# Performance work log

Hardware: AMD Instinct MI355X
Metric: run time of the kernel (lower is better)

Reference implementation:

```python
import jax, jax.numpy as jnp
from jax import lax
import numpy as np

B, T, U, M = 256, 256, 512, 64


def setup_inputs() -> dict:
    key = jax.random.key(0)
    ks = jax.random.split(key, 4)
    scale = 0.05
    return {
        "x": jax.random.normal(ks[0], (B, T, U), dtype=jnp.float32),
        "memory0": jnp.zeros((B, M * U), dtype=jnp.float32),
        "Wr": jax.random.normal(ks[1], (U, M + 1), dtype=jnp.float32) * scale,
        "br": jnp.zeros((M + 1,), dtype=jnp.float32),
        "Wt": jax.random.normal(ks[2], (U, U), dtype=jnp.float32) * scale,
        "bt": jnp.zeros((U,), dtype=jnp.float32),
        "Ww": jax.random.normal(ks[3], (U, M), dtype=jnp.float32) * scale,
        "bw": jnp.zeros((M,), dtype=jnp.float32),
    }


def reference(x, memory0, Wr, br, Wt, bt, Ww, bw):
    b, t, u = x.shape
    m = Ww.shape[1]
    mem0 = memory0.reshape(b, m, u)

    def step(mem, xt):
        # mem: [B, M, U], xt: [B, U]
        attended_mem = jnp.concatenate([mem, xt[:, None, :]], axis=1)  # [B, M+1, U]
        read_w = jax.nn.softmax(jnp.mean(attended_mem, axis=1) @ Wr + br, axis=-1)  # [B, M+1]
        attended = jnp.einsum('bm,bmu->bu', read_w, attended_mem)  # [B, U]
        transformed = jax.nn.relu(attended @ Wt + bt)  # [B, U]
        write_w = jax.nn.sigmoid(transformed @ Ww + bw)[:, :, None]  # [B, M, 1]
        mem = (1.0 - write_w) * mem + write_w * transformed[:, None, :]
        return mem, transformed

    _, outs = lax.scan(step, mem0, jnp.swapaxes(x, 0, 1))  # outs: [T, B, U]
    return jnp.swapaxes(outs, 0, 1)  # [B, T, U]
```

## Files before the change

### kernel.cpp

```cpp
#include <hip/hip_runtime.h>
#include <cstddef>

#define BB 256
#define TT 256
#define UU 512
#define MM 64
#define NT 512
#define NCACHE 12

typedef _Float16 h2 __attribute__((ext_vector_type(2)));
typedef unsigned int uint32;

#define NWTP (UU / 2 * UU)
#define NWWP (UU / 2 * MM)
#define NWRP (UU / 2 * MM)

__device__ __forceinline__ uint32 pkf(float lo, float hi) {
    h2 v; v[0] = (_Float16)lo; v[1] = (_Float16)hi;
    return __builtin_bit_cast(uint32, v);
}
__device__ __forceinline__ h2 toh2(uint32 u) { return __builtin_bit_cast(h2, u); }
__device__ __forceinline__ float fd2(uint32 wu, uint32 au, float acc) {
    return __builtin_amdgcn_fdot2(toh2(wu), toh2(au), acc, false);
}

__device__ __forceinline__ void bar() {
    asm volatile("s_waitcnt lgkmcnt(0)" ::: "memory");
    __builtin_amdgcn_s_barrier();
}
__device__ __forceinline__ void cfence() {
    asm volatile("" ::: "memory");
}

__global__ void cvt_kernel(const float* __restrict__ Wt,
                           const float* __restrict__ Wr,
                           const float* __restrict__ Ww,
                           uint32* __restrict__ Wtp,
                           uint32* __restrict__ Wwp,
                           uint32* __restrict__ Wrp) {
    int i = blockIdx.x * blockDim.x + threadIdx.x;
    const int n = NWTP + NWWP + NWRP;
    for (; i < n; i += gridDim.x * blockDim.x) {
        if (i < NWTP) {
            int k2 = i >> 9, r = i & 511;
            int jj = r >> 3, c = r & 7;
            int col = (c < 4) ? (jj * 4 + c) : (256 + jj * 4 + (c - 4));
            Wtp[i] = pkf(Wt[(size_t)(2 * k2) * UU + col],
                         Wt[(size_t)(2 * k2 + 1) * UU + col]);
        } else if (i < NWTP + NWWP) {
            int o = i - NWTP;
            int k2g = o >> 8, jj = (o >> 2) & 63, c = o & 3;
            int k2 = 4 * k2g + c;
            Wwp[o] = pkf(Ww[(size_t)(2 * k2) * MM + jj],
                         Ww[(size_t)(2 * k2 + 1) * MM + jj]);
        } else {
            int o = i - NWTP - NWWP;
            int k2g = o >> 8, jj = (o >> 2) & 63, c = o & 3;
            int k2 = 4 * k2g + c;
            Wrp[o] = pkf(Wr[(size_t)(2 * k2) * 65 + jj],
                         Wr[(size_t)(2 * k2 + 1) * 65 + jj]);
        }
    }
}

__global__ __launch_bounds__(NT, 1) void dnc_kernel(
    const float* __restrict__ x,
    const float* __restrict__ mem0,
    const float* __restrict__ Wr,
    const float* __restrict__ br,
    const float* __restrict__ bt,
    const float* __restrict__ bw,
    const uint32* __restrict__ Wtp,
    const uint32* __restrict__ Wwp,
    const uint32* __restrict__ Wrp,
    float* __restrict__ out)
{
    const int tid = threadIdx.x;
    const int b   = blockIdx.x;
    const int w   = tid >> 6;
    const int jj  = tid & 63;
    const int ut  = tid;

    __shared__ __align__(16) uint32 Wwl[NWWP];
    __shared__ __align__(16) uint32 Wrl[NWRP];
    __shared__ __align__(16) float  pWt[8][UU];
    __shared__ __align__(16) float  p1[8][68];
    __shared__ __align__(16) float  p2[8][68];
    __shared__ __align__(16) float  lds_rw[8][64];
    __shared__ __align__(16) float  lds_ww[8][64];
    __shared__ __align__(16) uint32 mean2[UU / 2];
    __shared__ __align__(16) uint32 att2[UU / 2];
    __shared__ __align__(16) uint32 tr2[UU / 2];

    const uint4* Wp4 = (const uint4*)Wtp;

    {
        const uint4* s1 = (const uint4*)Wwp;
        const uint4* s2 = (const uint4*)Wrp;
        uint4* d1 = (uint4*)Wwl;
        uint4* d2 = (uint4*)Wrl;
#pragma unroll
        for (int i = 0; i < 8; ++i) {
            d1[tid + i * 512] = s1[tid + i * 512];
            d2[tid + i * 512] = s2[tid + i * 512];
        }
    }

    uint4 wtcL[NCACHE], wtcH[NCACHE];
#pragma unroll
    for (int i = 0; i < NCACHE; ++i) {
        size_t base = (size_t)(w * 32 + i) * 128 + jj * 2;
        wtcL[i] = Wp4[base];
        wtcH[i] = Wp4[base + 1];
    }

    float memc[MM];
#pragma unroll
    for (int m = 0; m < MM; ++m)
        memc[m] = mem0[(size_t)b * (MM * UU) + (size_t)m * UU + ut];

    const float btv  = bt[ut];
    const float wr64 = Wr[(size_t)ut * 65 + 64];
    const float bw_j = bw[jj];
    const float br_j = br[jj];
    const float br64 = br[64];

    float tr_prev = 0.f;
    float xv = x[(size_t)b * TT * UU + ut];

    const uint4* Wwl4 = (const uint4*)Wwl;
    const uint4* Wrl4 = (const uint4*)Wrl;
    const uint4* t4   = (const uint4*)tr2;
    const uint4* m4   = (const uint4*)mean2;
    const uint4* a4   = (const uint4*)att2;

    __syncthreads();

    for (int t = 0; t < TT; ++t) {
        if (t > 0) {
            {
                float pa = 0.f, pb = 0.f;
#pragma unroll
                for (int g = 0; g < 8; ++g) {
                    uint4 W = Wwl4[(w * 8 + g) * 64 + jj];
                    uint4 T = t4[w * 8 + g];
                    pa = fd2(W.x, T.x, pa);
                    pb = fd2(W.y, T.y, pb);
                    pa = fd2(W.z, T.z, pa);
                    pb = fd2(W.w, T.w, pb);
                }
                p2[w][jj] = pa + pb;
            }
            bar();
            {
                float s = bw_j;
#pragma unroll
                for (int q = 0; q < 8; ++q) s += p2[q][jj];
                lds_ww[w][jj] = 1.f / (1.f + __expf(-s));
            }
            cfence();
#pragma unroll
            for (int q = 0; q < 16; ++q) {
                float4 wv = *(const float4*)&lds_ww[w][q * 4];
                memc[q*4+0] = (1.f - wv.x) * memc[q*4+0] + wv.x * tr_prev;
                memc[q*4+1] = (1.f - wv.y) * memc[q*4+1] + wv.y * tr_prev;
                memc[q*4+2] = (1.f - wv.z) * memc[q*4+2] + wv.z * tr_prev;
                memc[q*4+3] = (1.f - wv.w) * memc[q*4+3] + wv.w * tr_prev;
            }
        }

        {
            float c0 = 0.f, c1 = 0.f, c2 = 0.f, c3 = 0.f;
#pragma unroll
            for (int m = 0; m < MM; m += 4) {
                c0 += memc[m]; c1 += memc[m + 1];
                c2 += memc[m + 2]; c3 += memc[m + 3];
            }
            float meanv = ((c0 + c1) + (c2 + c3) + xv) * (1.f / 65.f);
            float mn = __shfl_down(meanv, 1, 64);
            if ((ut & 1) == 0) mean2[ut >> 1] = pkf(meanv, mn);
            float pv = meanv * wr64;
#pragma unroll
            for (int o = 32; o >= 1; o >>= 1) pv += __shfl_xor(pv, o, 64);
            if (jj == 0) p1[w][64] = pv;
        }
        bar();

        {
            float pa = 0.f, pb = 0.f;
#pragma unroll
            for (int g = 0; g < 8; ++g) {
                uint4 W = Wrl4[(w * 8 + g) * 64 + jj];
                uint4 M = m4[w * 8 + g];
                pa = fd2(W.x, M.x, pa);
                pb = fd2(W.y, M.y, pb);
                pa = fd2(W.z, M.z, pa);
                pb = fd2(W.w, M.w, pb);
            }
            p1[w][jj] = pa + pb;
        }
        bar();

        float rw64;
        {
            float lj = br_j;
#pragma unroll
            for (int q = 0; q < 8; ++q) lj += p1[q][jj];
            float s64 = br64;
#pragma unroll
            for (int q = 0; q < 8; ++q) s64 += p1[q][64];
            float l64 = s64;
            float mx = fmaxf(lj, l64);
#pragma unroll
            for (int o = 32; o >= 1; o >>= 1) mx = fmaxf(mx, __shfl_xor(mx, o, 64));
            float e = __expf(lj - mx);
            float e64 = __expf(l64 - mx);
            float sm = e;
#pragma unroll
            for (int o = 32; o >= 1; o >>= 1) sm += __shfl_xor(sm, o, 64);
            sm += e64;
            lds_rw[w][jj] = e / sm;
            rw64 = e64 / sm;
        }
        cfence();

        {
            float aa0 = rw64 * xv, aa1 = 0.f;
#pragma unroll
            for (int q = 0; q < 16; q += 2) {
                float4 r0 = *(const float4*)&lds_rw[w][q * 4];
                aa0 += r0.x * memc[q*4+0] + r0.y * memc[q*4+1]
                     + r0.z * memc[q*4+2] + r0.w * memc[q*4+3];
                float4 r1 = *(const float4*)&lds_rw[w][q * 4 + 4];
                aa1 += r1.x * memc[q*4+4] + r1.y * memc[q*4+5]
                     + r1.z * memc[q*4+6] + r1.w * memc[q*4+7];
            }
            float att = aa0 + aa1;
            float an = __shfl_down(att, 1, 64);
            if ((ut & 1) == 0) att2[ut >> 1] = pkf(att, an);
        }
        bar();

        {
            float acc[8];
#pragma unroll
            for (int c = 0; c < 8; ++c) acc[c] = 0.f;

            auto dot8 = [&](const uint4& L, const uint4& H, uint32 au) {
                acc[0] = fd2(L.x, au, acc[0]);
                acc[1] = fd2(L.y, au, acc[1]);
                acc[2] = fd2(L.z, au, acc[2]);
                acc[3] = fd2(L.w, au, acc[3]);
                acc[4] = fd2(H.x, au, acc[4]);
                acc[5] = fd2(H.y, au, acc[5]);
                acc[6] = fd2(H.z, au, acc[6]);
                acc[7] = fd2(H.w, au, acc[7]);
            };

            const uint4* sp = Wp4 + (size_t)(w * 32 + NCACHE) * 128 + jj * 2;
#pragma unroll 4
            for (int i = 0; i < 32 - NCACHE; ++i) {
                uint4 L = sp[(size_t)i * 128];
                uint4 H = sp[(size_t)i * 128 + 1];
                dot8(L, H, att2[w * 32 + NCACHE + i]);
            }
#pragma unroll
            for (int g = 0; g < NCACHE / 4; ++g) {
                uint4 A = a4[w * 8 + g];
                dot8(wtcL[4*g+0], wtcH[4*g+0], A.x);
                dot8(wtcL[4*g+1], wtcH[4*g+1], A.y);
                dot8(wtcL[4*g+2], wtcH[4*g+2], A.z);
                dot8(wtcL[4*g+3], wtcH[4*g+3], A.w);
            }

            *(float4*)&pWt[w][jj * 4]       = make_float4(acc[0], acc[1], acc[2], acc[3]);
            *(float4*)&pWt[w][256 + jj * 4] = make_float4(acc[4], acc[5], acc[6], acc[7]);
        }
        bar();

        {
            float s0 = 0.f, s1 = 0.f;
#pragma unroll
            for (int q = 0; q < 8; q += 2) {
                s0 += pWt[q][ut];
                s1 += pWt[q + 1][ut];
            }
            float tr = fmaxf(s0 + s1 + btv, 0.f);
            tr_prev = tr;
            out[(size_t)b * TT * UU + (size_t)t * UU + ut] = tr;
            float trn = __shfl_down(tr, 1, 64);
            if ((ut & 1) == 0) tr2[ut >> 1] = pkf(tr, trn);
        }

        {
            int tn = (t + 1 < TT) ? t + 1 : t;
            xv = x[(size_t)b * TT * UU + (size_t)tn * UU + ut];
        }
        bar();
    }
}

extern "C" void kernel_launch(void* const* d_in, const int* in_sizes, int n_in,
                              void* d_out, int out_size, void* d_ws, size_t ws_size,
                              hipStream_t stream) {
    const float* x    = (const float*)d_in[0];
    const float* mem0 = (const float*)d_in[1];
    const float* Wr   = (const float*)d_in[2];
    const float* br   = (const float*)d_in[3];
    const float* Wt   = (const float*)d_in[4];
    const float* bt   = (const float*)d_in[5];
    const float* Ww   = (const float*)d_in[6];
    const float* bw   = (const float*)d_in[7];
    float* out = (float*)d_out;

    uint32* Wtp = (uint32*)d_ws;
    uint32* Wwp = Wtp + NWTP;
    uint32* Wrp = Wwp + NWWP;

    cvt_kernel<<<dim3(256), dim3(256), 0, stream>>>(Wt, Wr, Ww, Wtp, Wwp, Wrp);
    dnc_kernel<<<dim3(BB), dim3(NT), 0, stream>>>(
        x, mem0, Wr, br, bt, bw, Wtp, Wwp, Wrp, out);
}
```

Measured before the change: 1.576 ms.

## Stage part of Wt in LDS and registers, read Ww/Wr from global

```diff
diff --git a/kernel.cpp b/kernel.cpp
--- a/kernel.cpp
+++ b/kernel.cpp
@@ -6,7 +6,8 @@
 #define UU 512
 #define MM 64
 #define NT 512
-#define NCACHE 12
+#define NCACHE 16
+#define NLDS   8
 
 typedef _Float16 h2 __attribute__((ext_vector_type(2)));
 typedef unsigned int uint32;
@@ -81,8 +82,8 @@
     const int jj  = tid & 63;
     const int ut  = tid;
 
-    __shared__ __align__(16) uint32 Wwl[NWWP];
-    __shared__ __align__(16) uint32 Wrl[NWRP];
+    __shared__ __align__(16) uint4  WtlL4[4096];
+    __shared__ __align__(16) uint4  WtlH4[4096];
     __shared__ __align__(16) float  pWt[8][UU];
     __shared__ __align__(16) float  p1[8][68];
     __shared__ __align__(16) float  p2[8][68];
@@ -92,17 +93,18 @@
     __shared__ __align__(16) uint32 att2[UU / 2];
     __shared__ __align__(16) uint32 tr2[UU / 2];
 
-    const uint4* Wp4 = (const uint4*)Wtp;
+    const uint4* Wp4  = (const uint4*)Wtp;
+    const uint4* Wwp4 = (const uint4*)Wwp;
+    const uint4* Wrp4 = (const uint4*)Wrp;
 
     {
-        const uint4* s1 = (const uint4*)Wwp;
-        const uint4* s2 = (const uint4*)Wrp;
-        uint4* d1 = (uint4*)Wwl;
-        uint4* d2 = (uint4*)Wrl;
 #pragma unroll
         for (int i = 0; i < 8; ++i) {
-            d1[tid + i * 512] = s1[tid + i * 512];
-            d2[tid + i * 512] = s2[tid + i * 512];
+            int l = tid + i * 512;
+            int w_ = l >> 9, kp = (l >> 6) & 7, j_ = l & 63;
+            size_t src = (size_t)(w_ * 32 + NCACHE + kp) * 128 + j_ * 2;
+            WtlL4[l] = Wp4[src];
+            WtlH4[l] = Wp4[src + 1];
         }
     }
 
@@ -128,11 +130,9 @@
     float tr_prev = 0.f;
     float xv = x[(size_t)b * TT * UU + ut];
 
-    const uint4* Wwl4 = (const uint4*)Wwl;
-    const uint4* Wrl4 = (const uint4*)Wrl;
-    const uint4* t4   = (const uint4*)tr2;
-    const uint4* m4   = (const uint4*)mean2;
-    const uint4* a4   = (const uint4*)att2;
+    const uint4* t4 = (const uint4*)tr2;
+    const uint4* m4 = (const uint4*)mean2;
+    const uint4* a4 = (const uint4*)att2;
 
     __syncthreads();
 
@@ -142,7 +142,7 @@
                 float pa = 0.f, pb = 0.f;
 #pragma unroll
                 for (int g = 0; g < 8; ++g) {
-                    uint4 W = Wwl4[(w * 8 + g) * 64 + jj];
+                    uint4 W = Wwp4[(w * 8 + g) * 64 + jj];
                     uint4 T = t4[w * 8 + g];
                     pa = fd2(W.x, T.x, pa);
                     pb = fd2(W.y, T.y, pb);
@@ -190,7 +190,7 @@
             float pa = 0.f, pb = 0.f;
 #pragma unroll
             for (int g = 0; g < 8; ++g) {
-                uint4 W = Wrl4[(w * 8 + g) * 64 + jj];
+                uint4 W = Wrp4[(w * 8 + g) * 64 + jj];
                 uint4 M = m4[w * 8 + g];
                 pa = fd2(W.x, M.x, pa);
                 pb = fd2(W.y, M.y, pb);
@@ -257,11 +257,17 @@
                 acc[7] = fd2(H.w, au, acc[7]);
             };
 
-            const uint4* sp = Wp4 + (size_t)(w * 32 + NCACHE) * 128 + jj * 2;
+            const uint4* sp = Wp4 + (size_t)(w * 32 + NCACHE + NLDS) * 128 + jj * 2;
 #pragma unroll 4
-            for (int i = 0; i < 32 - NCACHE; ++i) {
+            for (int i = 0; i < 32 - NCACHE - NLDS; ++i) {
                 uint4 L = sp[(size_t)i * 128];
                 uint4 H = sp[(size_t)i * 128 + 1];
+                dot8(L, H, att2[w * 32 + NCACHE + NLDS + i]);
+            }
+#pragma unroll
+            for (int i = 0; i < NLDS; ++i) {
+                uint4 L = WtlL4[w * 512 + i * 64 + jj];
+                uint4 H = WtlH4[w * 512 + i * 64 + jj];
                 dot8(L, H, att2[w * 32 + NCACHE + i]);
             }
 #pragma unroll
```

After: 2.304 ms. 1.46x slower.
